# Performance work log

Hardware: AMD Instinct MI355X
Metric: run time of the kernel (lower is better)

## Reference

```python
import jax, jax.numpy as jnp
from jax import lax
import numpy as np

NUM_ANCHORS = 3
NUM_CLASSES = 20
IMG_DIM = 416.0
ANCHORS = np.array([[10.0, 13.0], [16.0, 30.0], [33.0, 23.0]], dtype=np.float32)
BN_EPS = 1e-5


def setup_inputs() -> dict:
    key = jax.random.key(0)
    ks = jax.random.split(key, 8)
    B, Cin, G = 16, 256, 52
    Cmid = 2 * Cin
    Cout = NUM_ANCHORS * (NUM_CLASSES + 5)
    # weights scaled down so exp() in the box decode stays numerically tame
    return {
        "x": jax.random.normal(ks[0], (B, Cin, G, G), jnp.float32),
        "conv1_w": jax.random.normal(ks[1], (Cmid, Cin, 3, 3), jnp.float32) * 0.05,
        "bn_gamma": jnp.ones((Cmid,), jnp.float32),
        "bn_beta": jnp.zeros((Cmid,), jnp.float32),
        "bn_mean": jax.random.normal(ks[2], (Cmid,), jnp.float32) * 0.05,
        "bn_var": jax.random.uniform(ks[3], (Cmid,), jnp.float32, 0.5, 1.5),
        "conv2_w": jax.random.normal(ks[4], (Cout, Cmid, 1, 1), jnp.float32) * 0.05,
        "conv2_b": jnp.zeros((Cout,), jnp.float32),
    }


def _conv(x, w, padding):
    return lax.conv_general_dilated(
        x, w, window_strides=(1, 1), padding=padding,
        dimension_numbers=("NCHW", "OIHW", "NCHW"))


def reference(x, conv1_w, bn_gamma, bn_beta, bn_mean, bn_var, conv2_w, conv2_b):
    # BasicConv: conv3x3 (no bias) -> BatchNorm (inference stats) -> LeakyReLU(0.1)
    y = _conv(x, conv1_w, ((1, 1), (1, 1)))
    inv = bn_gamma / jnp.sqrt(bn_var + BN_EPS)
    y = y * inv[None, :, None, None] + (bn_beta - bn_mean * inv)[None, :, None, None]
    y = jnp.where(y > 0, y, 0.1 * y)
    # 1x1 head conv with bias
    y = _conv(y, conv2_w, ((0, 0), (0, 0))) + conv2_b[None, :, None, None]

    B, G = y.shape[0], y.shape[2]
    A, NC = NUM_ANCHORS, NUM_CLASSES
    # [B, A, 5+NC, G, G] -> [B, A, G, G, 5+NC]
    pred = y.reshape(B, A, NC + 5, G, G).transpose(0, 1, 3, 4, 2)

    obj_score = jax.nn.sigmoid(pred[..., 4])        # [B,A,G,G]
    pred_cls = jax.nn.sigmoid(pred[..., 5:])        # [B,A,G,G,NC]

    stride = IMG_DIM / G
    grid = jnp.arange(G, dtype=jnp.float32)
    grid_x = grid[None, None, None, :]              # [1,1,1,G]
    grid_y = grid[None, None, :, None]              # [1,1,G,1]
    scaled = jnp.asarray(ANCHORS) / stride          # [A,2]
    anchor_w = scaled[:, 0].reshape(1, A, 1, 1)
    anchor_h = scaled[:, 1].reshape(1, A, 1, 1)

    # original uses .data (detached) for box decode
    box_in = lax.stop_gradient(pred[..., :4])
    bx = jax.nn.sigmoid(box_in[..., 0]) + grid_x
    by = jax.nn.sigmoid(box_in[..., 1]) + grid_y
    bw = jnp.exp(box_in[..., 2]) * anchor_w
    bh = jnp.exp(box_in[..., 3]) * anchor_h
    pred_boxes = jnp.stack([bx, by, bw, bh], axis=-1) * stride  # [B,A,G,G,4]

    return jnp.concatenate(
        [pred_boxes.reshape(B, -1, 4),
         obj_score.reshape(B, -1, 1),
         pred_cls.reshape(B, -1, NC)], axis=-1)
```

## Files before the change

### kernel.cpp

```cpp
#include <hip/hip_runtime.h>

typedef _Float16 f16;
typedef _Float16 f16x8 __attribute__((ext_vector_type(8)));
typedef _Float16 f16x4 __attribute__((ext_vector_type(4)));
typedef float f32x4 __attribute__((ext_vector_type(4)));

#define GDIM 52
#define GG 2704
#define CIN 256
#define CMID 512
#define COUT 75
#define NIMG 16
#define SPT 192
#define NSPB 15
#define PH 60
#define PW 54

#define AT_OFF 0
#define AT_SZ 16384
#define SLAB_OFF 49152
#define SLAB_SZ 32768

__device__ __forceinline__ float sigmoidf_(float x) {
    return 1.0f / (1.0f + __expf(-x));
}

__device__ __forceinline__ void gload16(const void* g, void* l) {
    __builtin_amdgcn_global_load_lds(
        (const __attribute__((address_space(1))) unsigned int*)g,
        (__attribute__((address_space(3))) unsigned int*)l, 16, 0, 0);
}

__global__ __launch_bounds__(256) void k_prep_x(const float* __restrict__ x,
                                                f16* __restrict__ x16p) {
    __shared__ float ls[32][133];
    int hw0 = blockIdx.x * 128, ck = blockIdx.y, img = blockIdx.z;
    int tid = threadIdx.x;
    const float* xb = x + ((size_t)img * CIN + ck * 32) * GG;
#pragma unroll
    for (int i = 0; i < 16; ++i) {
        int idx = tid + i * 256;
        int r = idx >> 7, c = idx & 127;
        int hw = hw0 + c;
        ls[r][c] = (hw < GG) ? xb[(size_t)r * GG + hw] : 0.0f;
    }
    __syncthreads();
    int col = tid >> 1, half = tid & 1;
    int hw = hw0 + col;
    if (hw < GG) {
        int h = hw / GDIM, w = hw % GDIM;
        f16* dst = x16p + ((((size_t)img * 8 + ck) * PH + h + 1) * PW + (w + 1)) * 32 + half * 16;
        f16x8 o0, o1;
#pragma unroll
        for (int j = 0; j < 8; ++j) o0[j] = (f16)ls[half * 16 + j][col];
#pragma unroll
        for (int j = 0; j < 8; ++j) o1[j] = (f16)ls[half * 16 + 8 + j][col];
        *(f16x8*)dst = o0;
        *(f16x8*)(dst + 8) = o1;
    }
}

__global__ __launch_bounds__(256) void k_prep_w(
    const float* __restrict__ w1, const float* __restrict__ w2,
    const float* __restrict__ gamma, const float* __restrict__ beta,
    const float* __restrict__ mean, const float* __restrict__ var,
    f16* __restrict__ w16, f16* __restrict__ w2_16,
    float* __restrict__ bnscale, float* __restrict__ bnshift) {
    int i = blockIdx.x * 256 + threadIdx.x;
    int cl = i & 31;
    int co = (i >> 5) & 511;
    int ckt = i >> 14;
    int ck = ckt & 7, tap = ckt >> 3;
    int ci = ck * 32 + cl;
    w16[i] = (f16)w1[(size_t)co * 2304 + ci * 9 + tap];
    if (i < COUT * CMID) w2_16[i] = (f16)w2[i];
    if (i < CMID) {
        float s = gamma[i] * rsqrtf(var[i] + 1e-5f);
        bnscale[i] = s;
        bnshift[i] = beta[i] - mean[i] * s;
    }
}

__global__ __launch_bounds__(512, 2) void k_conv1(
    const f16* __restrict__ x16p, const f16* __restrict__ w16,
    const float* __restrict__ bnscale, const float* __restrict__ bnshift,
    f16* __restrict__ y16) {
    __shared__ __align__(16) char smem[114688];
    int img = blockIdx.x / NSPB, sb = blockIdx.x % NSPB;
    int n0 = sb * SPT;
    int h_lo = n0 / GDIM;
    int half = blockIdx.y;
    int co0 = half * 256;
    int tid = threadIdx.x;
    int lane = tid & 63, wave = tid >> 6;
    int wm = wave >> 1, wn = wave & 1;
    int l15 = lane & 15, kg = lane >> 4;

    int roff[6];
#pragma unroll
    for (int nf = 0; nf < 6; ++nf) {
        int n = n0 + wn * 96 + nf * 16 + l15;
        int nc = n < GG ? n : GG - 1;
        int hh = nc / GDIM, ww = nc % GDIM;
        roff[nf] = ((hh - h_lo + 1) * PW + (ww + 1)) * 8;
    }

    f32x4 acc[4][6];
#pragma unroll
    for (int a = 0; a < 4; ++a)
#pragma unroll
        for (int b = 0; b < 6; ++b) {
            acc[a][b][0] = 0.f; acc[a][b][1] = 0.f;
            acc[a][b][2] = 0.f; acc[a][b][3] = 0.f;
        }

    const f16* xbase = x16p + ((size_t)img * 8 * PH + h_lo) * (PW * 32);
    int spix = tid < 378 ? tid : 377;

    {
        const f16* wA = w16 + (size_t)co0 * 32;
        f16* dst = (f16*)(smem + AT_OFF);
#pragma unroll
        for (int p = 0; p < 2; ++p) {
            int u = p * 512 + tid, s = u >> 8, c = u & 255;
            gload16(wA + (size_t)c * 32 + s * 8, dst + (size_t)u * 8);
        }
        f16* sd = (f16*)(smem + SLAB_OFF);
#pragma unroll
        for (int p = 0; p < 4; ++p)
            gload16(xbase + (size_t)spix * 32 + p * 8, sd + ((size_t)p * 512 + tid) * 8);
    }

    for (int ck = 0; ck < 8; ++ck) {
#pragma unroll
        for (int tap = 0; tap < 9; ++tap) {
            if (!(ck == 7 && tap == 8)) {
                const int tapn = (tap + 1) % 9;
                const int ckn = ck + (tap == 8 ? 1 : 0);
                const f16* wA = w16 + ((size_t)(tapn * 8 + ckn) * 512 + co0) * 32;
                f16* dst = (f16*)(smem + AT_OFF + ((tap + 1) % 3) * AT_SZ);
#pragma unroll
                for (int p = 0; p < 2; ++p) {
                    int u = p * 512 + tid, s = u >> 8, c = u & 255;
                    gload16(wA + (size_t)c * 32 + s * 8, dst + (size_t)u * 8);
                }
            }
            if (tap == 4 && ck < 7) {
                const f16* sg = xbase + (size_t)(ck + 1) * (PH * PW * 32);
                f16* sd = (f16*)(smem + SLAB_OFF + ((ck + 1) & 1) * SLAB_SZ);
#pragma unroll
                for (int p = 0; p < 4; ++p)
                    gload16(sg + (size_t)spix * 32 + p * 8, sd + ((size_t)p * 512 + tid) * 8);
            }
            if (ck == 7 && tap == 8)
                asm volatile("s_waitcnt vmcnt(0)" ::: "memory");
            else if ((tap == 4 || tap == 5) && ck < 7)
                asm volatile("s_waitcnt vmcnt(6)" ::: "memory");
            else
                asm volatile("s_waitcnt vmcnt(2)" ::: "memory");
            __builtin_amdgcn_s_barrier();
            __builtin_amdgcn_sched_barrier(0);
            const f16* Ab = (const f16*)(smem + AT_OFF + (tap % 3) * AT_SZ);
            const f16* Sb = (const f16*)(smem + SLAB_OFF + (ck & 1) * SLAB_SZ);
            const int tappix = (tap / 3 - 1) * PW + (tap % 3 - 1);
            f16x8 af[4], bf[6];
#pragma unroll
            for (int mf = 0; mf < 4; ++mf)
                af[mf] = *(const f16x8*)(Ab + kg * 2048 + (wm * 64 + l15) * 8 + mf * 128);
#pragma unroll
            for (int nf = 0; nf < 6; ++nf)
                bf[nf] = *(const f16x8*)(Sb + kg * 4096 + roff[nf] + tappix * 8);
            __builtin_amdgcn_s_setprio(1);
#pragma unroll
            for (int nf = 0; nf < 6; ++nf)
#pragma unroll
                for (int mf = 0; mf < 4; ++mf)
                    acc[mf][nf] = __builtin_amdgcn_mfma_f32_16x16x32_f16(
                        af[mf], bf[nf], acc[mf][nf], 0, 0, 0);
            __builtin_amdgcn_s_setprio(0);
            __builtin_amdgcn_sched_barrier(0);
        }
    }
    __syncthreads();
    f16* tb = (f16*)smem;
#pragma unroll
    for (int mf = 0; mf < 4; ++mf) {
        int cr = wm * 64 + mf * 16 + kg * 4;
        f32x4 sc = *(const f32x4*)(bnscale + co0 + cr);
        f32x4 sh = *(const f32x4*)(bnshift + co0 + cr);
#pragma unroll
        for (int nf = 0; nf < 6; ++nf) {
            int pl = wn * 96 + nf * 16 + l15;
            f16x4 o;
#pragma unroll
            for (int i = 0; i < 4; ++i) {
                float v = acc[mf][nf][i] * sc[i] + sh[i];
                o[i] = (f16)(v > 0.f ? v : 0.1f * v);
            }
            *(f16x4*)(tb + pl * 264 + cr) = o;
        }
    }
    __syncthreads();
    int valid = GG - n0; if (valid > SPT) valid = SPT;
    f16* yb = y16 + (size_t)half * (NIMG * (size_t)GG * 256) + ((size_t)img * GG + n0) * 256;
#pragma unroll
    for (int p = 0; p < 12; ++p) {
        int u = p * 512 + tid, pl = u >> 5, slot = u & 31;
        if (pl < valid)
            *(f16x8*)(yb + (size_t)pl * 256 + slot * 8) =
                *(const f16x8*)(tb + pl * 264 + slot * 8);
    }
}

__global__ __launch_bounds__(256) void k_conv2(
    const f16* __restrict__ y16, const f16* __restrict__ w2_16,
    const float* __restrict__ b2, float* __restrict__ out) {
    __shared__ float ct[128][81];
    int img = blockIdx.x / 22, nb = blockIdx.x % 22;
    int n0 = nb * 128;
    int tid = threadIdx.x;
    int lane = tid & 63, wave = tid >> 6;
    int l15 = lane & 15, kg = lane >> 4;

    f32x4 acc[5][2];
#pragma unroll
    for (int a = 0; a < 5; ++a)
#pragma unroll
        for (int b = 0; b < 2; ++b) {
            acc[a][b][0] = 0.f; acc[a][b][1] = 0.f;
            acc[a][b][2] = 0.f; acc[a][b][3] = 0.f;
        }

    int nn[2];
#pragma unroll
    for (int nf = 0; nf < 2; ++nf) {
        int n = n0 + wave * 32 + nf * 16 + l15;
        nn[nf] = n < GG ? n : GG - 1;
    }
    for (int c0 = 0; c0 < CMID; c0 += 32) {
        const f16* yb = y16 + (size_t)(c0 >> 8) * (NIMG * (size_t)GG * 256) +
                        (size_t)img * GG * 256;
        int c = c0 & 255;
        f16x8 af[5];
#pragma unroll
        for (int mf = 0; mf < 5; ++mf) {
            int co = mf * 16 + l15;
            if (co < COUT)
                af[mf] = *(const f16x8*)(w2_16 + (size_t)co * CMID + c0 + kg * 8);
            else {
#pragma unroll
                for (int k = 0; k < 8; ++k) af[mf][k] = (f16)0;
            }
        }
#pragma unroll
        for (int nf = 0; nf < 2; ++nf) {
            f16x8 bf = *(const f16x8*)(yb + (size_t)nn[nf] * 256 + c + kg * 8);
#pragma unroll
            for (int mf = 0; mf < 5; ++mf)
                acc[mf][nf] = __builtin_amdgcn_mfma_f32_16x16x32_f16(
                    af[mf], bf, acc[mf][nf], 0, 0, 0);
        }
    }
#pragma unroll
    for (int mf = 0; mf < 5; ++mf)
#pragma unroll
        for (int nf = 0; nf < 2; ++nf)
            *(f32x4*)(&ct[wave * 32 + nf * 16 + l15][mf * 16 + kg * 4]) = acc[mf][nf];
    __syncthreads();
    for (int j = tid; j < 384; j += 256) {
        int a = j >> 7, nl = j & 127;
        int n = n0 + nl;
        if (n >= GG) continue;
        const float* t = &ct[nl][a * 25];
        float tv[25];
#pragma unroll
        for (int q = 0; q < 25; ++q) tv[q] = t[q] + b2[a * 25 + q];
        int h = n / GDIM, w = n % GDIM;
        const float AW[3] = {10.f, 16.f, 33.f};
        const float AH[3] = {13.f, 30.f, 23.f};
        float bx = (sigmoidf_(tv[0]) + (float)w) * 8.0f;
        float by = (sigmoidf_(tv[1]) + (float)h) * 8.0f;
        float bw_ = __expf(tv[2]) * AW[a];
        float bh_ = __expf(tv[3]) * AH[a];
        float* o = out + ((size_t)img * 8112 + (size_t)a * GG + n) * 25;
        o[0] = bx; o[1] = by; o[2] = bw_; o[3] = bh_;
        o[4] = sigmoidf_(tv[4]);
#pragma unroll
        for (int q = 0; q < 20; ++q) o[5 + q] = sigmoidf_(tv[5 + q]);
    }
}

extern "C" void kernel_launch(void* const* d_in, const int* in_sizes, int n_in,
                              void* d_out, int out_size, void* d_ws, size_t ws_size,
                              hipStream_t stream) {
    (void)in_sizes; (void)n_in; (void)out_size; (void)ws_size;
    const float* x     = (const float*)d_in[0];
    const float* w1    = (const float*)d_in[1];
    const float* gamma = (const float*)d_in[2];
    const float* beta  = (const float*)d_in[3];
    const float* mean  = (const float*)d_in[4];
    const float* var   = (const float*)d_in[5];
    const float* w2    = (const float*)d_in[6];
    const float* b2    = (const float*)d_in[7];
    float* out = (float*)d_out;

    char* ws = (char*)d_ws;
    f16* x16p     = (f16*)(ws);
    f16* w16      = (f16*)(ws + 26542080);
    f16* w2_16    = (f16*)(ws + 28901376);
    float* bnscale = (float*)(ws + 28978176);
    float* bnshift = (float*)(ws + 28980224);
    f16* y16      = (f16*)(ws + 28982272);

    hipMemsetAsync(x16p, 0, 26542080, stream);
    k_prep_x<<<dim3(22, 8, NIMG), 256, 0, stream>>>(x, x16p);
    k_prep_w<<<4608, 256, 0, stream>>>(w1, w2, gamma, beta, mean, var,
                                       w16, w2_16, bnscale, bnshift);
    k_conv1<<<dim3(NIMG * NSPB, 2), 512, 0, stream>>>(x16p, w16, bnscale,
                                                      bnshift, y16);
    k_conv2<<<NIMG * 22, 256, 0, stream>>>(y16, w2_16, b2, out);
}
```

Baseline: 155.4 us.

## Switch conv1 to 32x32x16 MFMA with 4 waves and register double-buffered fragments

Rewrites the conv1 main loop to use 32x32x16 MFMA tiles with 4 waves of 256 threads, each wave owning a 128x96 output tile instead of 64x96. LDS fragments for the next tap are prefetched into a second register set before the current MFMAs issue, overlapping LDS reads with compute. The full-buffer memset of the padded input is replaced by a small kernel that zeroes only the halo border. The trade-off is much higher register pressure per wave (large accumulators plus double-buffered fragments) and one block per CU. Halving the threads doubles the global-to-LDS load instructions each thread issues.

```diff
diff --git a/kernel.cpp b/kernel.cpp
--- a/kernel.cpp
+++ b/kernel.cpp
@@ -4,6 +4,7 @@
 typedef _Float16 f16x8 __attribute__((ext_vector_type(8)));
 typedef _Float16 f16x4 __attribute__((ext_vector_type(4)));
 typedef float f32x4 __attribute__((ext_vector_type(4)));
+typedef float f32x16 __attribute__((ext_vector_type(16)));
 
 #define GDIM 52
 #define GG 2704
@@ -21,6 +22,8 @@
 #define SLAB_OFF 49152
 #define SLAB_SZ 32768
 
+#define VMCNT(n) asm volatile("s_waitcnt vmcnt(" #n ")" ::: "memory")
+
 __device__ __forceinline__ float sigmoidf_(float x) {
     return 1.0f / (1.0f + __expf(-x));
 }
@@ -29,6 +32,22 @@
     __builtin_amdgcn_global_load_lds(
         (const __attribute__((address_space(1))) unsigned int*)g,
         (__attribute__((address_space(3))) unsigned int*)l, 16, 0, 0);
+}
+
+__global__ __launch_bounds__(256) void k_zero_border(f16* __restrict__ x16p) {
+    int ic = blockIdx.x;
+    int tid = threadIdx.x;
+    f16x8 z;
+#pragma unroll
+    for (int k = 0; k < 8; ++k) z[k] = (f16)0;
+    for (int j = tid; j < 536; j += 256) {
+        int row, col;
+        if (j < 432) { int r = j / 54; row = (r == 0) ? 0 : 52 + r; col = j % 54; }
+        else { int k = j - 432; row = 1 + (k >> 1); col = (k & 1) * 53; }
+        f16* p = x16p + (((size_t)ic * PH + row) * PW + col) * 32;
+#pragma unroll
+        for (int q = 0; q < 4; ++q) *(f16x8*)(p + q * 8) = z;
+    }
 }
 
 __global__ __launch_bounds__(256) void k_prep_x(const float* __restrict__ x,
@@ -81,7 +100,7 @@
     }
 }
 
-__global__ __launch_bounds__(512, 2) void k_conv1(
+__global__ __launch_bounds__(256, 1) void k_conv1(
     const f16* __restrict__ x16p, const f16* __restrict__ w16,
     const float* __restrict__ bnscale, const float* __restrict__ bnshift,
     f16* __restrict__ y16) {
@@ -94,118 +113,165 @@
     int tid = threadIdx.x;
     int lane = tid & 63, wave = tid >> 6;
     int wm = wave >> 1, wn = wave & 1;
-    int l15 = lane & 15, kg = lane >> 4;
-
-    int roff[6];
-#pragma unroll
-    for (int nf = 0; nf < 6; ++nf) {
-        int n = n0 + wn * 96 + nf * 16 + l15;
+    int l31 = lane & 31, hi = lane >> 5;
+
+    int roff[3];
+#pragma unroll
+    for (int nt = 0; nt < 3; ++nt) {
+        int n = n0 + wn * 96 + nt * 32 + l31;
         int nc = n < GG ? n : GG - 1;
         int hh = nc / GDIM, ww = nc % GDIM;
-        roff[nf] = ((hh - h_lo + 1) * PW + (ww + 1)) * 8;
-    }
-
-    f32x4 acc[4][6];
+        roff[nt] = ((hh - h_lo + 1) * PW + (ww + 1)) * 8;
+    }
+
+    f32x16 acc[4][3];
 #pragma unroll
     for (int a = 0; a < 4; ++a)
 #pragma unroll
-        for (int b = 0; b < 6; ++b) {
-            acc[a][b][0] = 0.f; acc[a][b][1] = 0.f;
-            acc[a][b][2] = 0.f; acc[a][b][3] = 0.f;
-        }
+        for (int b = 0; b < 3; ++b)
+#pragma unroll
+            for (int i = 0; i < 16; ++i) acc[a][b][i] = 0.f;
 
     const f16* xbase = x16p + ((size_t)img * 8 * PH + h_lo) * (PW * 32);
-    int spix = tid < 378 ? tid : 377;
+    f16x8 fa[2][8], fb[2][6];
 
     {
         const f16* wA = w16 + (size_t)co0 * 32;
         f16* dst = (f16*)(smem + AT_OFF);
 #pragma unroll
-        for (int p = 0; p < 2; ++p) {
-            int u = p * 512 + tid, s = u >> 8, c = u & 255;
-            gload16(wA + (size_t)c * 32 + s * 8, dst + (size_t)u * 8);
+        for (int p = 0; p < 4; ++p) {
+            int cix = p * 256 + tid;
+            gload16(wA + (size_t)(cix & 255) * 32 + (cix >> 8) * 8, dst + (size_t)cix * 8);
         }
         f16* sd = (f16*)(smem + SLAB_OFF);
 #pragma unroll
-        for (int p = 0; p < 4; ++p)
-            gload16(xbase + (size_t)spix * 32 + p * 8, sd + ((size_t)p * 512 + tid) * 8);
-    }
-
-    for (int ck = 0; ck < 8; ++ck) {
-#pragma unroll
-        for (int tap = 0; tap < 9; ++tap) {
-            if (!(ck == 7 && tap == 8)) {
-                const int tapn = (tap + 1) % 9;
-                const int ckn = ck + (tap == 8 ? 1 : 0);
+        for (int p = 0; p < 8; ++p) {
+            int cix = p * 256 + tid;
+            int pix = cix & 511; if (pix > 377) pix = 377;
+            gload16(xbase + (size_t)pix * 32 + (cix >> 9) * 8, sd + (size_t)cix * 8);
+        }
+        const f16* wA1 = w16 + ((size_t)(1 * 8 + 0) * 512 + co0) * 32;
+        f16* dst1 = (f16*)(smem + AT_OFF + AT_SZ);
+#pragma unroll
+        for (int p = 0; p < 4; ++p) {
+            int cix = p * 256 + tid;
+            gload16(wA1 + (size_t)(cix & 255) * 32 + (cix >> 8) * 8, dst1 + (size_t)cix * 8);
+        }
+    }
+    VMCNT(4);
+    __builtin_amdgcn_s_barrier();
+    __builtin_amdgcn_sched_barrier(0);
+    {
+        const f16* Ab = (const f16*)(smem + AT_OFF);
+        const f16* Sb = (const f16*)(smem + SLAB_OFF);
+        const int tappix = -PW - 1;
+#pragma unroll
+        for (int mt = 0; mt < 4; ++mt)
+#pragma unroll
+            for (int kh = 0; kh < 2; ++kh)
+                fa[0][mt * 2 + kh] = *(const f16x8*)(Ab + (kh * 2 + hi) * 2048 +
+                                                    (wm * 128 + mt * 32 + l31) * 8);
+#pragma unroll
+        for (int nt = 0; nt < 3; ++nt)
+#pragma unroll
+            for (int kh = 0; kh < 2; ++kh)
+                fb[0][nt * 2 + kh] = *(const f16x8*)(Sb + (kh * 2 + hi) * 4096 +
+                                                    roff[nt] + tappix * 8);
+    }
+    __builtin_amdgcn_sched_barrier(0);
+
+    for (int ck2 = 0; ck2 < 4; ++ck2) {
+#pragma unroll
+        for (int u = 0; u < 18; ++u) {
+            {
+                const int tapn = (u + 2) % 9;
+                int ckn = 2 * ck2 + (u + 2) / 9; if (ckn > 7) ckn = 7;
                 const f16* wA = w16 + ((size_t)(tapn * 8 + ckn) * 512 + co0) * 32;
-                f16* dst = (f16*)(smem + AT_OFF + ((tap + 1) % 3) * AT_SZ);
-#pragma unroll
-                for (int p = 0; p < 2; ++p) {
-                    int u = p * 512 + tid, s = u >> 8, c = u & 255;
-                    gload16(wA + (size_t)c * 32 + s * 8, dst + (size_t)u * 8);
+                f16* dst = (f16*)(smem + AT_OFF + ((u + 2) % 3) * AT_SZ);
+#pragma unroll
+                for (int p = 0; p < 4; ++p) {
+                    int cix = p * 256 + tid;
+                    gload16(wA + (size_t)(cix & 255) * 32 + (cix >> 8) * 8,
+                            dst + (size_t)cix * 8);
                 }
             }
-            if (tap == 4 && ck < 7) {
-                const f16* sg = xbase + (size_t)(ck + 1) * (PH * PW * 32);
-                f16* sd = (f16*)(smem + SLAB_OFF + ((ck + 1) & 1) * SLAB_SZ);
-#pragma unroll
-                for (int p = 0; p < 4; ++p)
-                    gload16(sg + (size_t)spix * 32 + p * 8, sd + ((size_t)p * 512 + tid) * 8);
-            }
-            if (ck == 7 && tap == 8)
-                asm volatile("s_waitcnt vmcnt(0)" ::: "memory");
-            else if ((tap == 4 || tap == 5) && ck < 7)
-                asm volatile("s_waitcnt vmcnt(6)" ::: "memory");
-            else
-                asm volatile("s_waitcnt vmcnt(2)" ::: "memory");
+            if (u == 1 || u == 10) {
+                const int sbuf = (u / 9 + 1) & 1;
+                int ckn = 2 * ck2 + u / 9 + 1; if (ckn > 7) ckn = 7;
+                const f16* sg = xbase + (size_t)ckn * (PH * PW * 32);
+                f16* sd = (f16*)(smem + SLAB_OFF + sbuf * SLAB_SZ);
+#pragma unroll
+                for (int p = 0; p < 8; ++p) {
+                    int cix = p * 256 + tid;
+                    int pix = cix & 511; if (pix > 377) pix = 377;
+                    gload16(sg + (size_t)pix * 32 + (cix >> 9) * 8, sd + (size_t)cix * 8);
+                }
+            }
+            if (u == 1 || u == 2 || u == 10 || u == 11) VMCNT(12); else VMCNT(4);
             __builtin_amdgcn_s_barrier();
             __builtin_amdgcn_sched_barrier(0);
-            const f16* Ab = (const f16*)(smem + AT_OFF + (tap % 3) * AT_SZ);
-            const f16* Sb = (const f16*)(smem + SLAB_OFF + (ck & 1) * SLAB_SZ);
-            const int tappix = (tap / 3 - 1) * PW + (tap % 3 - 1);
-            f16x8 af[4], bf[6];
-#pragma unroll
-            for (int mf = 0; mf < 4; ++mf)
-                af[mf] = *(const f16x8*)(Ab + kg * 2048 + (wm * 64 + l15) * 8 + mf * 128);
-#pragma unroll
-            for (int nf = 0; nf < 6; ++nf)
-                bf[nf] = *(const f16x8*)(Sb + kg * 4096 + roff[nf] + tappix * 8);
-            __builtin_amdgcn_s_setprio(1);
-#pragma unroll
-            for (int nf = 0; nf < 6; ++nf)
-#pragma unroll
-                for (int mf = 0; mf < 4; ++mf)
-                    acc[mf][nf] = __builtin_amdgcn_mfma_f32_16x16x32_f16(
-                        af[mf], bf[nf], acc[mf][nf], 0, 0, 0);
-            __builtin_amdgcn_s_setprio(0);
+            if (!(u == 17 && ck2 == 3)) {
+                const int un = u + 1;
+                const f16* Ab = (const f16*)(smem + AT_OFF + (un % 3) * AT_SZ);
+                const f16* Sb = (const f16*)(smem + SLAB_OFF + ((un / 9) & 1) * SLAB_SZ);
+                const int tapn = un % 9;
+                const int tappix = (tapn / 3 - 1) * PW + (tapn % 3 - 1);
+#pragma unroll
+                for (int mt = 0; mt < 4; ++mt)
+#pragma unroll
+                    for (int kh = 0; kh < 2; ++kh)
+                        fa[un & 1][mt * 2 + kh] =
+                            *(const f16x8*)(Ab + (kh * 2 + hi) * 2048 +
+                                            (wm * 128 + mt * 32 + l31) * 8);
+#pragma unroll
+                for (int nt = 0; nt < 3; ++nt)
+#pragma unroll
+                    for (int kh = 0; kh < 2; ++kh)
+                        fb[un & 1][nt * 2 + kh] =
+                            *(const f16x8*)(Sb + (kh * 2 + hi) * 4096 +
+                                            roff[nt] + tappix * 8);
+            }
             __builtin_amdgcn_sched_barrier(0);
-        }
-    }
+#pragma unroll
+            for (int kh = 0; kh < 2; ++kh)
+#pragma unroll
+                for (int nt = 0; nt < 3; ++nt)
+#pragma unroll
+                    for (int mt = 0; mt < 4; ++mt)
+                        acc[mt][nt] = __builtin_amdgcn_mfma_f32_32x32x16_f16(
+                            fa[u & 1][mt * 2 + kh], fb[u & 1][nt * 2 + kh],
+                            acc[mt][nt], 0, 0, 0);
+            __builtin_amdgcn_sched_barrier(0);
+        }
+    }
+    VMCNT(0);
     __syncthreads();
     f16* tb = (f16*)smem;
 #pragma unroll
-    for (int mf = 0; mf < 4; ++mf) {
-        int cr = wm * 64 + mf * 16 + kg * 4;
-        f32x4 sc = *(const f32x4*)(bnscale + co0 + cr);
-        f32x4 sh = *(const f32x4*)(bnshift + co0 + cr);
-#pragma unroll
-        for (int nf = 0; nf < 6; ++nf) {
-            int pl = wn * 96 + nf * 16 + l15;
-            f16x4 o;
-#pragma unroll
-            for (int i = 0; i < 4; ++i) {
-                float v = acc[mf][nf][i] * sc[i] + sh[i];
-                o[i] = (f16)(v > 0.f ? v : 0.1f * v);
-            }
-            *(f16x4*)(tb + pl * 264 + cr) = o;
-        }
-    }
+    for (int mt = 0; mt < 4; ++mt)
+#pragma unroll
+        for (int q = 0; q < 4; ++q) {
+            int co_l = wm * 128 + mt * 32 + q * 8 + hi * 4;
+            f32x4 sc = *(const f32x4*)(bnscale + co0 + co_l);
+            f32x4 sh = *(const f32x4*)(bnshift + co0 + co_l);
+#pragma unroll
+            for (int nt = 0; nt < 3; ++nt) {
+                int pix_l = wn * 96 + nt * 32 + l31;
+                f16x4 o;
+#pragma unroll
+                for (int i = 0; i < 4; ++i) {
+                    float v = acc[mt][nt][q * 4 + i] * sc[i] + sh[i];
+                    o[i] = (f16)(v > 0.f ? v : 0.1f * v);
+                }
+                *(f16x4*)(tb + pix_l * 264 + co_l) = o;
+            }
+        }
     __syncthreads();
     int valid = GG - n0; if (valid > SPT) valid = SPT;
     f16* yb = y16 + (size_t)half * (NIMG * (size_t)GG * 256) + ((size_t)img * GG + n0) * 256;
 #pragma unroll
-    for (int p = 0; p < 12; ++p) {
-        int u = p * 512 + tid, pl = u >> 5, slot = u & 31;
+    for (int p = 0; p < 24; ++p) {
+        int u = p * 256 + tid, pl = u >> 5, slot = u & 31;
         if (pl < valid)
             *(f16x8*)(yb + (size_t)pl * 256 + slot * 8) =
                 *(const f16x8*)(tb + pl * 264 + slot * 8);
@@ -312,11 +378,11 @@
     float* bnshift = (float*)(ws + 28980224);
     f16* y16      = (f16*)(ws + 28982272);
 
-    hipMemsetAsync(x16p, 0, 26542080, stream);
+    k_zero_border<<<NIMG * 8, 256, 0, stream>>>(x16p);
     k_prep_x<<<dim3(22, 8, NIMG), 256, 0, stream>>>(x, x16p);
     k_prep_w<<<4608, 256, 0, stream>>>(w1, w2, gamma, beta, mean, var,
                                        w16, w2_16, bnscale, bnshift);
-    k_conv1<<<dim3(NIMG * NSPB, 2), 512, 0, stream>>>(x16p, w16, bnscale,
+    k_conv1<<<dim3(NIMG * NSPB, 2), 256, 0, stream>>>(x16p, w16, bnscale,
                                                       bnshift, y16);
     k_conv2<<<NIMG * 22, 256, 0, stream>>>(y16, w2_16, b2, out);
 }
```

New measurement: 168.0 us. 1.08x slower.

## Prefetch LDS fragments one step ahead and replace full memset with border zeroing

Applied to the files above, without the earlier changes.

The conv1 main loop is restructured into 72 flat steps. It uses a 4-deep weight ring in LDS (a larger shared allocation) and prefetches the next step's A/B fragments into registers while the current step's MFMAs issue. This hides LDS read latency behind the matrix math. The slab load layout is also changed to be channel-chunk-major. The full 26 MB memset of the padded input buffer is replaced by a small kernel that zeroes only the halo border. The costs are more registers and LDS, which may limit occupancy at two blocks per CU, plus a risk of wrong indexing at the last steps.

```diff
diff --git a/kernel.cpp b/kernel.cpp
--- a/kernel.cpp
+++ b/kernel.cpp
@@ -18,8 +18,10 @@
 
 #define AT_OFF 0
 #define AT_SZ 16384
-#define SLAB_OFF 49152
+#define SLAB_OFF 65536
 #define SLAB_SZ 32768
+
+#define VMCNT(n) asm volatile("s_waitcnt vmcnt(" #n ")" ::: "memory")
 
 __device__ __forceinline__ float sigmoidf_(float x) {
     return 1.0f / (1.0f + __expf(-x));
@@ -29,6 +31,22 @@
     __builtin_amdgcn_global_load_lds(
         (const __attribute__((address_space(1))) unsigned int*)g,
         (__attribute__((address_space(3))) unsigned int*)l, 16, 0, 0);
+}
+
+__global__ __launch_bounds__(256) void k_zero_border(f16* __restrict__ x16p) {
+    int ic = blockIdx.x;
+    int tid = threadIdx.x;
+    f16x8 z;
+#pragma unroll
+    for (int k = 0; k < 8; ++k) z[k] = (f16)0;
+    for (int j = tid; j < 536; j += 256) {
+        int row, col;
+        if (j < 432) { int r = j / 54; row = (r == 0) ? 0 : 52 + r; col = j % 54; }
+        else { int k = j - 432; row = 1 + (k >> 1); col = (k & 1) * 53; }
+        f16* p = x16p + (((size_t)ic * PH + row) * PW + col) * 32;
+#pragma unroll
+        for (int q = 0; q < 4; ++q) *(f16x8*)(p + q * 8) = z;
+    }
 }
 
 __global__ __launch_bounds__(256) void k_prep_x(const float* __restrict__ x,
@@ -85,7 +103,7 @@
     const f16* __restrict__ x16p, const f16* __restrict__ w16,
     const float* __restrict__ bnscale, const float* __restrict__ bnshift,
     f16* __restrict__ y16) {
-    __shared__ __align__(16) char smem[114688];
+    __shared__ __align__(16) char smem[131072];
     int img = blockIdx.x / NSPB, sb = blockIdx.x % NSPB;
     int n0 = sb * SPT;
     int h_lo = n0 / GDIM;
@@ -115,68 +133,105 @@
         }
 
     const f16* xbase = x16p + ((size_t)img * 8 * PH + h_lo) * (PW * 32);
-    int spix = tid < 378 ? tid : 377;
+    f16x8 fa[2][4], fb[2][6];
 
     {
-        const f16* wA = w16 + (size_t)co0 * 32;
-        f16* dst = (f16*)(smem + AT_OFF);
+        const f16* wA0 = w16 + (size_t)co0 * 32;
+        f16* d0 = (f16*)(smem + AT_OFF);
 #pragma unroll
         for (int p = 0; p < 2; ++p) {
             int u = p * 512 + tid, s = u >> 8, c = u & 255;
-            gload16(wA + (size_t)c * 32 + s * 8, dst + (size_t)u * 8);
+            gload16(wA0 + (size_t)c * 32 + s * 8, d0 + (size_t)u * 8);
         }
         f16* sd = (f16*)(smem + SLAB_OFF);
 #pragma unroll
-        for (int p = 0; p < 4; ++p)
-            gload16(xbase + (size_t)spix * 32 + p * 8, sd + ((size_t)p * 512 + tid) * 8);
-    }
-
-    for (int ck = 0; ck < 8; ++ck) {
-#pragma unroll
-        for (int tap = 0; tap < 9; ++tap) {
-            if (!(ck == 7 && tap == 8)) {
-                const int tapn = (tap + 1) % 9;
-                const int ckn = ck + (tap == 8 ? 1 : 0);
-                const f16* wA = w16 + ((size_t)(tapn * 8 + ckn) * 512 + co0) * 32;
-                f16* dst = (f16*)(smem + AT_OFF + ((tap + 1) % 3) * AT_SZ);
+        for (int p = 0; p < 4; ++p) {
+            int cix = p * 512 + tid;
+            int pix = cix & 511; if (pix > 377) pix = 377;
+            gload16(xbase + (size_t)pix * 32 + (cix >> 9) * 8, sd + (size_t)cix * 8);
+        }
+        const f16* wA1 = w16 + ((size_t)8 * 512 + co0) * 32;
+        f16* d1 = (f16*)(smem + AT_OFF + AT_SZ);
+#pragma unroll
+        for (int p = 0; p < 2; ++p) {
+            int u = p * 512 + tid, s = u >> 8, c = u & 255;
+            gload16(wA1 + (size_t)c * 32 + s * 8, d1 + (size_t)u * 8);
+        }
+    }
+    VMCNT(2);
+    __builtin_amdgcn_s_barrier();
+    __builtin_amdgcn_sched_barrier(0);
+    {
+        const f16* Ab = (const f16*)(smem + AT_OFF);
+        const f16* Sb = (const f16*)(smem + SLAB_OFF);
+        const int tappix = -PW - 1;
+#pragma unroll
+        for (int mf = 0; mf < 4; ++mf)
+            fa[0][mf] = *(const f16x8*)(Ab + kg * 2048 + (wm * 64 + l15) * 8 + mf * 128);
+#pragma unroll
+        for (int nf = 0; nf < 6; ++nf)
+            fb[0][nf] = *(const f16x8*)(Sb + kg * 4096 + roff[nf] + tappix * 8);
+    }
+    __builtin_amdgcn_sched_barrier(0);
+
+    for (int q = 0; q < 2; ++q) {
+#pragma unroll
+        for (int u = 0; u < 36; ++u) {
+            if (u == 1 || u == 10 || u == 19 || u == 28) {
+                int ckS = q * 4 + u / 9 + 1;
+                const f16* sg;
+                f16* sd;
+                if (ckS > 7) {
+                    sg = xbase + (size_t)7 * (PH * PW * 32);
+                    sd = (f16*)(smem + AT_OFF + ((u + 2) % 4) * AT_SZ);
+                } else {
+                    sg = xbase + (size_t)ckS * (PH * PW * 32);
+                    sd = (f16*)(smem + SLAB_OFF + (((u / 9) + 1) & 1) * SLAB_SZ);
+                }
+#pragma unroll
+                for (int p = 0; p < 4; ++p) {
+                    int cix = p * 512 + tid;
+                    int pix = cix & 511; if (pix > 377) pix = 377;
+                    gload16(sg + (size_t)pix * 32 + (cix >> 9) * 8, sd + (size_t)cix * 8);
+                }
+            }
+            {
+                const int tap2 = (u + 2) % 9;
+                int ckA = q * 4 + (u + 2) / 9; if (ckA > 7) ckA = 7;
+                const f16* wA = w16 + ((size_t)(tap2 * 8 + ckA) * 512 + co0) * 32;
+                f16* dst = (f16*)(smem + AT_OFF + ((u + 2) % 4) * AT_SZ);
 #pragma unroll
                 for (int p = 0; p < 2; ++p) {
-                    int u = p * 512 + tid, s = u >> 8, c = u & 255;
-                    gload16(wA + (size_t)c * 32 + s * 8, dst + (size_t)u * 8);
+                    int uu = p * 512 + tid, s = uu >> 8, c = uu & 255;
+                    gload16(wA + (size_t)c * 32 + s * 8, dst + (size_t)uu * 8);
                 }
             }
-            if (tap == 4 && ck < 7) {
-                const f16* sg = xbase + (size_t)(ck + 1) * (PH * PW * 32);
-                f16* sd = (f16*)(smem + SLAB_OFF + ((ck + 1) & 1) * SLAB_SZ);
-#pragma unroll
-                for (int p = 0; p < 4; ++p)
-                    gload16(sg + (size_t)spix * 32 + p * 8, sd + ((size_t)p * 512 + tid) * 8);
-            }
-            if (ck == 7 && tap == 8)
-                asm volatile("s_waitcnt vmcnt(0)" ::: "memory");
-            else if ((tap == 4 || tap == 5) && ck < 7)
-                asm volatile("s_waitcnt vmcnt(6)" ::: "memory");
-            else
-                asm volatile("s_waitcnt vmcnt(2)" ::: "memory");
+            if (u == 1 || u == 10 || u == 19 || u == 28) VMCNT(6); else VMCNT(2);
             __builtin_amdgcn_s_barrier();
             __builtin_amdgcn_sched_barrier(0);
-            const f16* Ab = (const f16*)(smem + AT_OFF + (tap % 3) * AT_SZ);
-            const f16* Sb = (const f16*)(smem + SLAB_OFF + (ck & 1) * SLAB_SZ);
-            const int tappix = (tap / 3 - 1) * PW + (tap % 3 - 1);
-            f16x8 af[4], bf[6];
-#pragma unroll
-            for (int mf = 0; mf < 4; ++mf)
-                af[mf] = *(const f16x8*)(Ab + kg * 2048 + (wm * 64 + l15) * 8 + mf * 128);
-#pragma unroll
-            for (int nf = 0; nf < 6; ++nf)
-                bf[nf] = *(const f16x8*)(Sb + kg * 4096 + roff[nf] + tappix * 8);
+            {
+                const int un = u + 1;
+                const f16* Ab = (const f16*)(smem + AT_OFF + (un % 4) * AT_SZ);
+                const f16* Sb = (const f16*)(smem + SLAB_OFF + ((un / 9) & 1) * SLAB_SZ);
+                const int tapn = un % 9;
+                const int tappix = (tapn / 3 - 1) * PW + (tapn % 3 - 1);
+#pragma unroll
+                for (int mf = 0; mf < 4; ++mf)
+                    fa[un & 1][mf] = *(const f16x8*)(Ab + kg * 2048 +
+                                                    (wm * 64 + l15) * 8 + mf * 128);
+#pragma unroll
+                for (int nf = 0; nf < 6; ++nf)
+                    fb[un & 1][nf] = *(const f16x8*)(Sb + kg * 4096 +
+                                                    roff[nf] + tappix * 8);
+            }
+            __builtin_amdgcn_sched_barrier(0);
             __builtin_amdgcn_s_setprio(1);
 #pragma unroll
             for (int nf = 0; nf < 6; ++nf)
 #pragma unroll
                 for (int mf = 0; mf < 4; ++mf)
                     acc[mf][nf] = __builtin_amdgcn_mfma_f32_16x16x32_f16(
-                        af[mf], bf[nf], acc[mf][nf], 0, 0, 0);
+                        fa[u & 1][mf], fb[u & 1][nf], acc[mf][nf], 0, 0, 0);
             __builtin_amdgcn_s_setprio(0);
             __builtin_amdgcn_sched_barrier(0);
         }
@@ -312,7 +367,7 @@
     float* bnshift = (float*)(ws + 28980224);
     f16* y16      = (f16*)(ws + 28982272);
 
-    hipMemsetAsync(x16p, 0, 26542080, stream);
+    k_zero_border<<<NIMG * 8, 256, 0, stream>>>(x16p);
     k_prep_x<<<dim3(22, 8, NIMG), 256, 0, stream>>>(x, x16p);
     k_prep_w<<<4608, 256, 0, stream>>>(w1, w2, gamma, beta, mean, var,
                                        w16, w2_16, bnscale, bnshift);
```

Measured after the change: 167.6 us. 1.08x slower.

## Group conv1 taps into three-tap phases with register double-buffering and zero only borders

Applied to the files above, without the earlier changes.

The conv1 main loop now stages three weight taps per barrier phase, double-buffered in a larger LDS region. Fragment reads are interleaved with MFMAs across two register sets, which cuts barriers and waitcnt stalls from nine per channel chunk to three. The input slab is trimmed to the 384 pixels actually needed. The full memset of the padded input buffer is replaced by a small kernel that zeroes only the padding border, avoiding a ~26MB write. The risks are the larger LDS footprint, more registers held, and full vmcnt(0) waits in each phase.

```diff
diff --git a/kernel.cpp b/kernel.cpp
--- a/kernel.cpp
+++ b/kernel.cpp
@@ -16,10 +16,12 @@
 #define PH 60
 #define PW 54
 
-#define AT_OFF 0
-#define AT_SZ 16384
-#define SLAB_OFF 49152
-#define SLAB_SZ 32768
+#define AG_OFF 0
+#define AG_SZ 49152
+#define SLAB_OFF 98304
+#define SLAB_SZ 24576
+
+#define VMCNT0 asm volatile("s_waitcnt vmcnt(0)" ::: "memory")
 
 __device__ __forceinline__ float sigmoidf_(float x) {
     return 1.0f / (1.0f + __expf(-x));
@@ -29,6 +31,22 @@
     __builtin_amdgcn_global_load_lds(
         (const __attribute__((address_space(1))) unsigned int*)g,
         (__attribute__((address_space(3))) unsigned int*)l, 16, 0, 0);
+}
+
+__global__ __launch_bounds__(256) void k_zero_border(f16* __restrict__ x16p) {
+    int ic = blockIdx.x;
+    int tid = threadIdx.x;
+    f16x8 z;
+#pragma unroll
+    for (int k = 0; k < 8; ++k) z[k] = (f16)0;
+    for (int j = tid; j < 536; j += 256) {
+        int row, col;
+        if (j < 432) { int r = j / 54; row = (r == 0) ? 0 : 52 + r; col = j % 54; }
+        else { int k = j - 432; row = 1 + (k >> 1); col = (k & 1) * 53; }
+        f16* p = x16p + (((size_t)ic * PH + row) * PW + col) * 32;
+#pragma unroll
+        for (int q = 0; q < 4; ++q) *(f16x8*)(p + q * 8) = z;
+    }
 }
 
 __global__ __launch_bounds__(256) void k_prep_x(const float* __restrict__ x,
@@ -81,11 +99,41 @@
     }
 }
 
+#define RD(aa, bb, JJ, TAPC)                                                   \
+    do {                                                                       \
+        const f16* Ab_ = Ag + (JJ) * 8192;                                     \
+        const int TPX_ = (((TAPC) / 3 - 1) * PW + ((TAPC) % 3) - 1) * 8;       \
+        aa##0 = *(const f16x8*)(Ab_ + a_lane);                                 \
+        aa##1 = *(const f16x8*)(Ab_ + a_lane + 128);                           \
+        aa##2 = *(const f16x8*)(Ab_ + a_lane + 256);                           \
+        aa##3 = *(const f16x8*)(Ab_ + a_lane + 384);                           \
+        bb##0 = *(const f16x8*)(Sb + kgx + roff[0] + TPX_);                    \
+        bb##1 = *(const f16x8*)(Sb + kgx + roff[1] + TPX_);                    \
+        bb##2 = *(const f16x8*)(Sb + kgx + roff[2] + TPX_);                    \
+        bb##3 = *(const f16x8*)(Sb + kgx + roff[3] + TPX_);                    \
+        bb##4 = *(const f16x8*)(Sb + kgx + roff[4] + TPX_);                    \
+        bb##5 = *(const f16x8*)(Sb + kgx + roff[5] + TPX_);                    \
+    } while (0)
+
+#define MM1(aa, bb, NF)                                                        \
+    do {                                                                       \
+        acc[0][NF] = __builtin_amdgcn_mfma_f32_16x16x32_f16(aa##0, bb##NF, acc[0][NF], 0, 0, 0); \
+        acc[1][NF] = __builtin_amdgcn_mfma_f32_16x16x32_f16(aa##1, bb##NF, acc[1][NF], 0, 0, 0); \
+        acc[2][NF] = __builtin_amdgcn_mfma_f32_16x16x32_f16(aa##2, bb##NF, acc[2][NF], 0, 0, 0); \
+        acc[3][NF] = __builtin_amdgcn_mfma_f32_16x16x32_f16(aa##3, bb##NF, acc[3][NF], 0, 0, 0); \
+    } while (0)
+
+#define MM(aa, bb)                                                             \
+    do {                                                                       \
+        MM1(aa, bb, 0); MM1(aa, bb, 1); MM1(aa, bb, 2);                        \
+        MM1(aa, bb, 3); MM1(aa, bb, 4); MM1(aa, bb, 5);                        \
+    } while (0)
+
 __global__ __launch_bounds__(512, 2) void k_conv1(
     const f16* __restrict__ x16p, const f16* __restrict__ w16,
     const float* __restrict__ bnscale, const float* __restrict__ bnshift,
     f16* __restrict__ y16) {
-    __shared__ __align__(16) char smem[114688];
+    __shared__ __align__(16) char smem[147456];
     int img = blockIdx.x / NSPB, sb = blockIdx.x % NSPB;
     int n0 = sb * SPT;
     int h_lo = n0 / GDIM;
@@ -95,6 +143,8 @@
     int lane = tid & 63, wave = tid >> 6;
     int wm = wave >> 1, wn = wave & 1;
     int l15 = lane & 15, kg = lane >> 4;
+    int a_lane = kg * 2048 + (wm * 64 + l15) * 8;
+    int kgx = kg * 3072;
 
     int roff[6];
 #pragma unroll
@@ -115,72 +165,73 @@
         }
 
     const f16* xbase = x16p + ((size_t)img * 8 * PH + h_lo) * (PW * 32);
-    int spix = tid < 378 ? tid : 377;
-
+    f16x8 A0_0, A0_1, A0_2, A0_3, B0_0, B0_1, B0_2, B0_3, B0_4, B0_5;
+    f16x8 A1_0, A1_1, A1_2, A1_3, B1_0, B1_1, B1_2, B1_3, B1_4, B1_5;
+
+#pragma unroll
+    for (int j = 0; j < 3; ++j) {
+        const f16* wA = w16 + ((size_t)(j * 8) * 512 + co0) * 32;
+        f16* dst = (f16*)(smem + AG_OFF) + j * 8192;
+#pragma unroll
+        for (int p = 0; p < 2; ++p) {
+            int u = p * 512 + tid;
+            gload16(wA + (size_t)(u & 255) * 32 + (u >> 8) * 8, dst + (size_t)u * 8);
+        }
+    }
     {
-        const f16* wA = w16 + (size_t)co0 * 32;
-        f16* dst = (f16*)(smem + AT_OFF);
-#pragma unroll
-        for (int p = 0; p < 2; ++p) {
-            int u = p * 512 + tid, s = u >> 8, c = u & 255;
-            gload16(wA + (size_t)c * 32 + s * 8, dst + (size_t)u * 8);
-        }
         f16* sd = (f16*)(smem + SLAB_OFF);
 #pragma unroll
-        for (int p = 0; p < 4; ++p)
-            gload16(xbase + (size_t)spix * 32 + p * 8, sd + ((size_t)p * 512 + tid) * 8);
+        for (int p = 0; p < 3; ++p) {
+            int c = p * 512 + tid;
+            int s = c / 384, pix = c % 384;
+            gload16(xbase + (size_t)pix * 32 + s * 8, sd + (size_t)c * 8);
+        }
     }
 
     for (int ck = 0; ck < 8; ++ck) {
 #pragma unroll
-        for (int tap = 0; tap < 9; ++tap) {
-            if (!(ck == 7 && tap == 8)) {
-                const int tapn = (tap + 1) % 9;
-                const int ckn = ck + (tap == 8 ? 1 : 0);
-                const f16* wA = w16 + ((size_t)(tapn * 8 + ckn) * 512 + co0) * 32;
-                f16* dst = (f16*)(smem + AT_OFF + ((tap + 1) % 3) * AT_SZ);
-#pragma unroll
-                for (int p = 0; p < 2; ++p) {
-                    int u = p * 512 + tid, s = u >> 8, c = u & 255;
-                    gload16(wA + (size_t)c * 32 + s * 8, dst + (size_t)u * 8);
+        for (int ph = 0; ph < 3; ++ph) {
+            const int g = ck * 3 + ph;
+            VMCNT0;
+            __builtin_amdgcn_s_barrier();
+            __builtin_amdgcn_sched_barrier(0);
+            if (g < 23) {
+                const int ckn = (ph == 2) ? ck + 1 : ck;
+                const int phn = (ph == 2) ? 0 : ph + 1;
+                f16* dst = (f16*)(smem + AG_OFF + ((g + 1) & 1) * AG_SZ);
+#pragma unroll
+                for (int j = 0; j < 3; ++j) {
+                    const f16* wA =
+                        w16 + ((size_t)((phn * 3 + j) * 8 + ckn) * 512 + co0) * 32;
+#pragma unroll
+                    for (int p = 0; p < 2; ++p) {
+                        int u = p * 512 + tid;
+                        gload16(wA + (size_t)(u & 255) * 32 + (u >> 8) * 8,
+                                dst + (size_t)(j * 8192 + u * 8));
+                    }
                 }
             }
-            if (tap == 4 && ck < 7) {
+            if (ph == 1 && ck < 7) {
                 const f16* sg = xbase + (size_t)(ck + 1) * (PH * PW * 32);
                 f16* sd = (f16*)(smem + SLAB_OFF + ((ck + 1) & 1) * SLAB_SZ);
 #pragma unroll
-                for (int p = 0; p < 4; ++p)
-                    gload16(sg + (size_t)spix * 32 + p * 8, sd + ((size_t)p * 512 + tid) * 8);
+                for (int p = 0; p < 3; ++p) {
+                    int c = p * 512 + tid;
+                    int s = c / 384, pix = c % 384;
+                    gload16(sg + (size_t)pix * 32 + s * 8, sd + (size_t)c * 8);
+                }
             }
-            if (ck == 7 && tap == 8)
-                asm volatile("s_waitcnt vmcnt(0)" ::: "memory");
-            else if ((tap == 4 || tap == 5) && ck < 7)
-                asm volatile("s_waitcnt vmcnt(6)" ::: "memory");
-            else
-                asm volatile("s_waitcnt vmcnt(2)" ::: "memory");
-            __builtin_amdgcn_s_barrier();
-            __builtin_amdgcn_sched_barrier(0);
-            const f16* Ab = (const f16*)(smem + AT_OFF + (tap % 3) * AT_SZ);
+            const f16* Ag = (const f16*)(smem + AG_OFF + (g & 1) * AG_SZ);
             const f16* Sb = (const f16*)(smem + SLAB_OFF + (ck & 1) * SLAB_SZ);
-            const int tappix = (tap / 3 - 1) * PW + (tap % 3 - 1);
-            f16x8 af[4], bf[6];
-#pragma unroll
-            for (int mf = 0; mf < 4; ++mf)
-                af[mf] = *(const f16x8*)(Ab + kg * 2048 + (wm * 64 + l15) * 8 + mf * 128);
-#pragma unroll
-            for (int nf = 0; nf < 6; ++nf)
-                bf[nf] = *(const f16x8*)(Sb + kg * 4096 + roff[nf] + tappix * 8);
-            __builtin_amdgcn_s_setprio(1);
-#pragma unroll
-            for (int nf = 0; nf < 6; ++nf)
-#pragma unroll
-                for (int mf = 0; mf < 4; ++mf)
-                    acc[mf][nf] = __builtin_amdgcn_mfma_f32_16x16x32_f16(
-                        af[mf], bf[nf], acc[mf][nf], 0, 0, 0);
-            __builtin_amdgcn_s_setprio(0);
-            __builtin_amdgcn_sched_barrier(0);
-        }
-    }
+            RD(A0_, B0_, 0, ph * 3 + 0);
+            RD(A1_, B1_, 1, ph * 3 + 1);
+            MM(A0_, B0_);
+            RD(A0_, B0_, 2, ph * 3 + 2);
+            MM(A1_, B1_);
+            MM(A0_, B0_);
+        }
+    }
+    VMCNT0;
     __syncthreads();
     f16* tb = (f16*)smem;
 #pragma unroll
@@ -312,7 +363,7 @@
     float* bnshift = (float*)(ws + 28980224);
     f16* y16      = (f16*)(ws + 28982272);
 
-    hipMemsetAsync(x16p, 0, 26542080, stream);
+    k_zero_border<<<NIMG * 8, 256, 0, stream>>>(x16p);
     k_prep_x<<<dim3(22, 8, NIMG), 256, 0, stream>>>(x, x16p);
     k_prep_w<<<4608, 256, 0, stream>>>(w1, w2, gamma, beta, mean, var,
                                        w16, w2_16, bnscale, bnshift);
```

Result: slower. 161.3 us (+3.8%).
